# Optimization experiments

Hardware: AMD Instinct MI355X
Metric: run time of the kernel (lower is better)

The kernel has to match this reference:

```python
import jax, jax.numpy as jnp
import numpy as np

SPREAD, DEPTH, IN, OUT, B = 2, 12, 128, 128, 16


def _build_index(spread, depth):
    # Full tree, BFS indexing: node v has parent (v-1)//spread, children spread*v+1..spread*v+spread.
    # Index n_nodes is the padding (None) node; root's parent and leaf children point to it.
    n = (spread ** (depth + 1) - 1) // (spread - 1)
    tab = np.zeros((n + 1, spread + 2), dtype=np.int64)
    for v in range(n):
        tab[v, 0] = v
        tab[v, 1] = (v - 1) // spread if v > 0 else n
        first = spread * v + 1
        if first < n:
            tab[v, 2:] = np.arange(first, first + spread)
        else:
            tab[v, 2:] = n
    # row n (the None/padding node) stays all zeros, matching the original code
    return jnp.asarray(tab)


def setup_inputs() -> dict:
    key = jax.random.key(0)
    k1, k2 = jax.random.split(key)
    n = (SPREAD ** (DEPTH + 1) - 1) // (SPREAD - 1)  # 8191
    x = jax.random.normal(k1, (B, n + 1, IN), dtype=jnp.float32)
    mask = jax.random.uniform(k2, (SPREAD + 2, IN, OUT), minval=-0.5, maxval=0.5, dtype=jnp.float32)
    bias = jnp.zeros((OUT,), dtype=jnp.float32)
    return {"x": x, "mask": mask, "bias": bias, "index_tensor": _build_index(SPREAD, DEPTH)}


def reference(x, mask, bias, index_tensor):
    # gather self/parent/children features: [B, L, spread+2, in]
    g = x[:, index_tensor, :]
    # per-relation matmul, flattened over (relation, in) == matmul(flatten(g,2,3), flatten(mask,0,1))
    # NOTE: original adds only bias[-1] (scalar) because of bias[None, None, -1] indexing
    y = jnp.einsum('blki,kio->blo', g, mask) + bias[-1]
    return jax.nn.relu(y)
```

## Files before the change

### kernel.cpp

```cpp
#include <hip/hip_runtime.h>
#include <hip/hip_bf16.h>


namespace {

constexpr int kNodes = 8192;
constexpr int kIn = 128;
constexpr int kOut = 128;
constexpr int kThreads = 256;
constexpr int kGrid = 512;
constexpr int kPhases = 8;

typedef __attribute__((ext_vector_type(8))) short short8;
typedef __attribute__((ext_vector_type(4))) float f32x4;

__device__ short8 g_bfrag[16 * 8 * 64];
__device__ __align__(16) short g_xbf[16 * kNodes * kIn];

__device__ __forceinline__ short f2bf(float f) {
  return __builtin_bit_cast(short, __float2bfloat16(f));
}

template <int N>
__device__ __forceinline__ void waitvm() {
  asm volatile("s_waitcnt vmcnt(%0)" ::"n"(N) : "memory");
  __builtin_amdgcn_sched_barrier(0);
}
__device__ __forceinline__ void barrier() {
  __builtin_amdgcn_s_barrier();
  __builtin_amdgcn_sched_barrier(0);
}

__global__ void prep_bfrag(const float* __restrict__ mask) {
  const int t = blockIdx.x * blockDim.x + threadIdx.x;
  const int kk = t >> 9, g = (t >> 6) & 7, lane = t & 63;
  const int krow = kk * 32 + (lane >> 4) * 8;
  const int col = g * 16 + (lane & 15);
  short8 pk;
#pragma unroll
  for (int e = 0; e < 8; ++e) pk[e] = f2bf(mask[(krow + e) * kOut + col]);
  g_bfrag[t] = pk;
}

__global__ __launch_bounds__(256)
void cvt_x(const float* __restrict__ x) {
  const size_t t = (size_t)blockIdx.x * 256 + threadIdx.x;
  const f32x4 a = reinterpret_cast<const f32x4*>(x)[2 * t];
  const f32x4 b = reinterpret_cast<const f32x4*>(x)[2 * t + 1];
  short8 pk;
  pk[0] = f2bf(a[0]); pk[1] = f2bf(a[1]); pk[2] = f2bf(a[2]); pk[3] = f2bf(a[3]);
  pk[4] = f2bf(b[0]); pk[5] = f2bf(b[1]); pk[6] = f2bf(b[2]); pk[7] = f2bf(b[3]);
  reinterpret_cast<short8*>(g_xbf)[t] = pk;
}

__global__ __launch_bounds__(kThreads, 2)
void tree_gemm(const float* __restrict__ bias, float* __restrict__ y) {
  __shared__ __align__(16) short ldsA[2][32 * 512];

  const int tid  = threadIdx.x;
  const int lane = tid & 63;
  const int wv   = tid >> 6;
  const int l15  = lane & 15;
  const int l4   = lane >> 4;
  const int nbh  = lane >> 4;

  const float blast = bias[kOut - 1];

  const int sb = (blockIdx.x & 7) * (kGrid / 8) + (blockIdx.x >> 3);
  const int bb = sb >> 5;
  const int blockRow0 = (sb & 31) * 256;
  const short* xbf = g_xbf + (size_t)bb * kNodes * kIn;

  auto stage = [&](int p, int bufsel) {
    const int r0 = blockRow0 + p * 32;
#pragma unroll
    for (int j = 0; j < 8; ++j) {
      const int rho = wv * 8 + j;
      const int v = r0 + rho;
      const int par = (v > 0) ? ((v - 1) >> 1) : (kNodes - 1);
      const int f = 2 * v + 1;
      const int ch = (f < kNodes - 1) ? (f + (nbh & 1)) : (kNodes - 1);
      int gi = (nbh == 0) ? v : (nbh == 1) ? par : ch;
      if (v == kNodes - 1) gi = 0;
      const short* src = xbf + (size_t)gi * kIn + (((lane & 15) ^ (rho & 7)) << 3);
      const short* dst = &ldsA[bufsel][rho * 512];
      __builtin_amdgcn_global_load_lds(
          (const __attribute__((address_space(1))) void*)src,
          (__attribute__((address_space(3))) void*)dst, 16, 0, 0);
    }
  };

  const short8* gb = g_bfrag + wv * 2 * 64 + lane;

  auto compute = [&](int p) {
    const short* buf = ldsA[p & 1];
    f32x4 acc00 = {}, acc01 = {}, acc10 = {}, acc11 = {};
#pragma unroll
    for (int kk = 0; kk < 16; ++kk) {
      const short8 b0 = gb[kk * 512];
      const short8 b1 = gb[kk * 512 + 64];
      const int slot = (kk * 4 + l4) ^ (l15 & 7);
      const short8 a0 = *reinterpret_cast<const short8*>(buf + l15 * 512 + slot * 8);
      const short8 a1 = *reinterpret_cast<const short8*>(buf + (16 + l15) * 512 + slot * 8);
      acc00 = __builtin_amdgcn_mfma_f32_16x16x32_bf16(a0, b0, acc00, 0, 0, 0);
      acc01 = __builtin_amdgcn_mfma_f32_16x16x32_bf16(a0, b1, acc01, 0, 0, 0);
      acc10 = __builtin_amdgcn_mfma_f32_16x16x32_bf16(a1, b0, acc10, 0, 0, 0);
      acc11 = __builtin_amdgcn_mfma_f32_16x16x32_bf16(a1, b1, acc11, 0, 0, 0);
    }
    const int r0 = blockRow0 + p * 32;
    float* yb = y + ((size_t)bb * kNodes + r0) * kOut;
    const int oc = wv * 32 + l15;
#pragma unroll
    for (int r = 0; r < 4; ++r) {
      const int row = l4 * 4 + r;
      const float v00 = acc00[r] + blast, v01 = acc01[r] + blast;
      const float v10 = acc10[r] + blast, v11 = acc11[r] + blast;
      yb[row * kOut + oc]             = v00 > 0.f ? v00 : 0.f;
      yb[row * kOut + oc + 16]        = v01 > 0.f ? v01 : 0.f;
      yb[(16 + row) * kOut + oc]      = v10 > 0.f ? v10 : 0.f;
      yb[(16 + row) * kOut + oc + 16] = v11 > 0.f ? v11 : 0.f;
    }
  };

  stage(0, 0);
  stage(1, 1);
  for (int p = 0; p < kPhases; ++p) {
    waitvm<8>();
    barrier();
    compute(p);
    barrier();
    if (p + 2 < kPhases) stage(p + 2, p & 1);
  }
}

}

extern "C" void kernel_launch(void* const* d_in, const int* in_sizes, int n_in,
                              void* d_out, int out_size, void* d_ws, size_t ws_size,
                              hipStream_t stream) {
  const float* x    = (const float*)d_in[0];
  const float* mask = (const float*)d_in[1];
  const float* bias = (const float*)d_in[2];
  float*       y    = (float*)d_out;
  (void)in_sizes; (void)n_in; (void)out_size; (void)d_ws; (void)ws_size;

  prep_bfrag<<<dim3(32), dim3(256), 0, stream>>>(mask);
  cvt_x<<<dim3(8192), dim3(256), 0, stream>>>(x);
  tree_gemm<<<dim3(kGrid), dim3(kThreads), 0, stream>>>(bias, y);
}
```

Baseline: 57.37 us.

## Fuse fp32-to-bf16 conversion into gathered GEMM, staging fp32 rows per relation

Removes the separate pass that converted x to a bf16 copy, and instead gathers fp32 rows directly into LDS and converts them to bf16 in registers before the MFMAs. Staging is split so each phase loads one relation (self, parent, child0, child1) for 32 rows, accumulating across four phases. Grid and phase count double and occupancy hint rises to 4 blocks per CU. This avoids writing and re-reading a full bf16 copy of x, but the gather now moves twice as many bytes per element and adds conversion ALU work in the inner loop.

```diff
diff --git a/kernel.cpp b/kernel.cpp
--- a/kernel.cpp
+++ b/kernel.cpp
@@ -8,14 +8,13 @@
 constexpr int kIn = 128;
 constexpr int kOut = 128;
 constexpr int kThreads = 256;
-constexpr int kGrid = 512;
-constexpr int kPhases = 8;
+constexpr int kGrid = 1024;
+constexpr int kPhases = 16;
 
 typedef __attribute__((ext_vector_type(8))) short short8;
 typedef __attribute__((ext_vector_type(4))) float f32x4;
 
 __device__ short8 g_bfrag[16 * 8 * 64];
-__device__ __align__(16) short g_xbf[16 * kNodes * kIn];
 
 __device__ __forceinline__ short f2bf(float f) {
   return __builtin_bit_cast(short, __float2bfloat16(f));
@@ -42,48 +41,46 @@
   g_bfrag[t] = pk;
 }
 
-__global__ __launch_bounds__(256)
-void cvt_x(const float* __restrict__ x) {
-  const size_t t = (size_t)blockIdx.x * 256 + threadIdx.x;
-  const f32x4 a = reinterpret_cast<const f32x4*>(x)[2 * t];
-  const f32x4 b = reinterpret_cast<const f32x4*>(x)[2 * t + 1];
-  short8 pk;
-  pk[0] = f2bf(a[0]); pk[1] = f2bf(a[1]); pk[2] = f2bf(a[2]); pk[3] = f2bf(a[3]);
-  pk[4] = f2bf(b[0]); pk[5] = f2bf(b[1]); pk[6] = f2bf(b[2]); pk[7] = f2bf(b[3]);
-  reinterpret_cast<short8*>(g_xbf)[t] = pk;
-}
-
-__global__ __launch_bounds__(kThreads, 2)
-void tree_gemm(const float* __restrict__ bias, float* __restrict__ y) {
-  __shared__ __align__(16) short ldsA[2][32 * 512];
+__global__ __launch_bounds__(kThreads, 4)
+void tree_gemm(const float* __restrict__ x, const float* __restrict__ bias,
+               float* __restrict__ y) {
+  __shared__ __align__(16) float ldsA[2][32 * kIn];
 
   const int tid  = threadIdx.x;
   const int lane = tid & 63;
   const int wv   = tid >> 6;
   const int l15  = lane & 15;
   const int l4   = lane >> 4;
-  const int nbh  = lane >> 4;
+  const int lh   = lane >> 5;
+  const int l31  = lane & 31;
 
   const float blast = bias[kOut - 1];
 
   const int sb = (blockIdx.x & 7) * (kGrid / 8) + (blockIdx.x >> 3);
-  const int bb = sb >> 5;
-  const int blockRow0 = (sb & 31) * 256;
-  const short* xbf = g_xbf + (size_t)bb * kNodes * kIn;
+  const int bb = sb >> 6;
+  const int blockRow0 = (sb & 63) * 128;
+  const float* xb = x + (size_t)bb * kNodes * kIn;
 
   auto stage = [&](int p, int bufsel) {
-    const int r0 = blockRow0 + p * 32;
+    const int rg = p >> 2, kq = p & 3;
+    const int r0 = blockRow0 + rg * 32;
 #pragma unroll
-    for (int j = 0; j < 8; ++j) {
-      const int rho = wv * 8 + j;
-      const int v = r0 + rho;
-      const int par = (v > 0) ? ((v - 1) >> 1) : (kNodes - 1);
-      const int f = 2 * v + 1;
-      const int ch = (f < kNodes - 1) ? (f + (nbh & 1)) : (kNodes - 1);
-      int gi = (nbh == 0) ? v : (nbh == 1) ? par : ch;
+    for (int j = 0; j < 4; ++j) {
+      const int i   = wv * 4 + j;
+      const int row = 2 * i + lh;
+      const int v   = r0 + row;
+      int gi;
+      if (kq == 0) {
+        gi = v;
+      } else if (kq == 1) {
+        gi = (v > 0) ? ((v - 1) >> 1) : (kNodes - 1);
+      } else {
+        const int f = 2 * v + 1;
+        gi = (f < kNodes - 1) ? (f + (kq - 2)) : (kNodes - 1);
+      }
       if (v == kNodes - 1) gi = 0;
-      const short* src = xbf + (size_t)gi * kIn + (((lane & 15) ^ (rho & 7)) << 3);
-      const short* dst = &ldsA[bufsel][rho * 512];
+      const float* src = xb + (size_t)gi * kIn + ((l31 ^ (row & 7)) << 2);
+      float* dst = &ldsA[bufsel][i * 256];
       __builtin_amdgcn_global_load_lds(
           (const __attribute__((address_space(1))) void*)src,
           (__attribute__((address_space(3))) void*)dst, 16, 0, 0);
@@ -92,42 +89,61 @@
 
   const short8* gb = g_bfrag + wv * 2 * 64 + lane;
 
-  auto compute = [&](int p) {
-    const short* buf = ldsA[p & 1];
-    f32x4 acc00 = {}, acc01 = {}, acc10 = {}, acc11 = {};
-#pragma unroll
-    for (int kk = 0; kk < 16; ++kk) {
-      const short8 b0 = gb[kk * 512];
-      const short8 b1 = gb[kk * 512 + 64];
-      const int slot = (kk * 4 + l4) ^ (l15 & 7);
-      const short8 a0 = *reinterpret_cast<const short8*>(buf + l15 * 512 + slot * 8);
-      const short8 a1 = *reinterpret_cast<const short8*>(buf + (16 + l15) * 512 + slot * 8);
-      acc00 = __builtin_amdgcn_mfma_f32_16x16x32_bf16(a0, b0, acc00, 0, 0, 0);
-      acc01 = __builtin_amdgcn_mfma_f32_16x16x32_bf16(a0, b1, acc01, 0, 0, 0);
-      acc10 = __builtin_amdgcn_mfma_f32_16x16x32_bf16(a1, b0, acc10, 0, 0, 0);
-      acc11 = __builtin_amdgcn_mfma_f32_16x16x32_bf16(a1, b1, acc11, 0, 0, 0);
-    }
-    const int r0 = blockRow0 + p * 32;
-    float* yb = y + ((size_t)bb * kNodes + r0) * kOut;
-    const int oc = wv * 32 + l15;
-#pragma unroll
-    for (int r = 0; r < 4; ++r) {
-      const int row = l4 * 4 + r;
-      const float v00 = acc00[r] + blast, v01 = acc01[r] + blast;
-      const float v10 = acc10[r] + blast, v11 = acc11[r] + blast;
-      yb[row * kOut + oc]             = v00 > 0.f ? v00 : 0.f;
-      yb[row * kOut + oc + 16]        = v01 > 0.f ? v01 : 0.f;
-      yb[(16 + row) * kOut + oc]      = v10 > 0.f ? v10 : 0.f;
-      yb[(16 + row) * kOut + oc + 16] = v11 > 0.f ? v11 : 0.f;
-    }
-  };
+  const f32x4 vzero = {};
+  f32x4 a00 = {}, a01 = {}, a10 = {}, a11 = {};
 
   stage(0, 0);
   stage(1, 1);
+
   for (int p = 0; p < kPhases; ++p) {
-    waitvm<8>();
+    waitvm<4>();
     barrier();
-    compute(p);
+
+    const float* buf = ldsA[p & 1];
+    const int kq = p & 3;
+    if (kq == 0) { a00 = vzero; a01 = vzero; a10 = vzero; a11 = vzero; }
+
+#pragma unroll
+    for (int kk = 0; kk < 4; ++kk) {
+      const int kkg = kq * 4 + kk;
+      const short8 b0 = gb[kkg * 512];
+      const short8 b1 = gb[kkg * 512 + 64];
+      const int q  = kk * 8 + l4 * 2;
+      const int s0 = q ^ (l15 & 7);
+      const int s1 = (q + 1) ^ (l15 & 7);
+      const float* r0p = buf + l15 * kIn;
+      const float* r1p = buf + (16 + l15) * kIn;
+      const f32x4 lo0 = *reinterpret_cast<const f32x4*>(r0p + s0 * 4);
+      const f32x4 hi0 = *reinterpret_cast<const f32x4*>(r0p + s1 * 4);
+      const f32x4 lo1 = *reinterpret_cast<const f32x4*>(r1p + s0 * 4);
+      const f32x4 hi1 = *reinterpret_cast<const f32x4*>(r1p + s1 * 4);
+      short8 fa0, fa1;
+      fa0[0] = f2bf(lo0[0]); fa0[1] = f2bf(lo0[1]); fa0[2] = f2bf(lo0[2]); fa0[3] = f2bf(lo0[3]);
+      fa0[4] = f2bf(hi0[0]); fa0[5] = f2bf(hi0[1]); fa0[6] = f2bf(hi0[2]); fa0[7] = f2bf(hi0[3]);
+      fa1[0] = f2bf(lo1[0]); fa1[1] = f2bf(lo1[1]); fa1[2] = f2bf(lo1[2]); fa1[3] = f2bf(lo1[3]);
+      fa1[4] = f2bf(hi1[0]); fa1[5] = f2bf(hi1[1]); fa1[6] = f2bf(hi1[2]); fa1[7] = f2bf(hi1[3]);
+      a00 = __builtin_amdgcn_mfma_f32_16x16x32_bf16(fa0, b0, a00, 0, 0, 0);
+      a01 = __builtin_amdgcn_mfma_f32_16x16x32_bf16(fa0, b1, a01, 0, 0, 0);
+      a10 = __builtin_amdgcn_mfma_f32_16x16x32_bf16(fa1, b0, a10, 0, 0, 0);
+      a11 = __builtin_amdgcn_mfma_f32_16x16x32_bf16(fa1, b1, a11, 0, 0, 0);
+    }
+
+    if (kq == 3) {
+      const int r0 = blockRow0 + (p >> 2) * 32;
+      float* yb = y + ((size_t)bb * kNodes + r0) * kOut;
+      const int oc = wv * 32 + l15;
+#pragma unroll
+      for (int r = 0; r < 4; ++r) {
+        const int row = l4 * 4 + r;
+        const float v00 = a00[r] + blast, v01 = a01[r] + blast;
+        const float v10 = a10[r] + blast, v11 = a11[r] + blast;
+        yb[row * kOut + oc]             = v00 > 0.f ? v00 : 0.f;
+        yb[row * kOut + oc + 16]        = v01 > 0.f ? v01 : 0.f;
+        yb[(16 + row) * kOut + oc]      = v10 > 0.f ? v10 : 0.f;
+        yb[(16 + row) * kOut + oc + 16] = v11 > 0.f ? v11 : 0.f;
+      }
+    }
+
     barrier();
     if (p + 2 < kPhases) stage(p + 2, p & 1);
   }
@@ -145,6 +161,5 @@
   (void)in_sizes; (void)n_in; (void)out_size; (void)d_ws; (void)ws_size;
 
   prep_bfrag<<<dim3(32), dim3(256), 0, stream>>>(mask);
-  cvt_x<<<dim3(8192), dim3(256), 0, stream>>>(x);
-  tree_gemm<<<dim3(kGrid), dim3(kThreads), 0, stream>>>(bias, y);
+  tree_gemm<<<dim3(kGrid), dim3(kThreads), 0, stream>>>(x, bias, y);
 }
```

Measured after the change: 51.39 us. -10.4%, faster.
